# Kernel tuning notes

Measured on AMD Instinct MI355X. Metric: run time of the kernel, lower is better.

The kernel has to match this reference:

```python
import jax, jax.numpy as jnp
import numpy as np

HEAD_NUMS = 8
LN_EPS = 1e-5


def _layernorm(x, g, b):
    m = jnp.mean(x, axis=-1, keepdims=True)
    v = jnp.var(x, axis=-1, keepdims=True)
    return (x - m) * jax.lax.rsqrt(v + LN_EPS) * g + b


def setup_inputs() -> dict:
    key = jax.random.key(0)
    ks = jax.random.split(key, 6)
    B, S, D = 4, 2048, 512
    x = jax.random.normal(ks[0], (B, S, D), dtype=jnp.float32)
    W1 = jax.random.normal(ks[1], (4 * D, D), dtype=jnp.float32) * 0.02
    b1 = jnp.zeros((4 * D,), dtype=jnp.float32)
    ln_g = jnp.ones((D,), dtype=jnp.float32)
    ln_b = jnp.zeros((D,), dtype=jnp.float32)
    W2 = jax.random.normal(ks[2], (D, D), dtype=jnp.float32) * 0.02
    b2 = jnp.zeros((D,), dtype=jnp.float32)
    return {"x": x, "W1": W1, "b1": b1, "ln_g": ln_g, "ln_b": ln_b, "W2": W2, "b2": b2}


def reference(x, W1, b1, ln_g, ln_b, W2, b2):
    B, S, D = x.shape
    H = HEAD_NUMS
    hd = D // H
    # fused qkv+gate projection with SiLU (HSTU style)
    h = jax.nn.silu(x @ W1.T + b1)                   # [B,S,4D]
    h = h.reshape(B, S, 4, H, hd)                    # split into gate,q,k,v
    gate = jnp.transpose(h[:, :, 0], (0, 2, 1, 3))   # [B,H,S,hd]
    q = jnp.transpose(h[:, :, 1], (0, 2, 1, 3))
    k = jnp.transpose(h[:, :, 2], (0, 2, 1, 3))
    v = jnp.transpose(h[:, :, 3], (0, 2, 1, 3))
    scale = 1.0 / np.sqrt(hd).astype(np.float32)
    scores = jnp.einsum('bhsd,bhtd->bhst', q, k) * scale   # [B,H,S,S]
    causal = jnp.tril(jnp.ones((S, S), dtype=bool))        # allowed: t <= s
    # silu replaces softmax; masked (future) positions contribute 0
    # (mathematical limit of silu(-inf) is 0)
    a = jnp.where(causal, jax.nn.silu(scores), 0.0)
    o = jnp.einsum('bhst,bhtd->bhsd', a, v)                # [B,H,S,hd]
    o = jnp.transpose(o, (0, 2, 1, 3)).reshape(B, S, D)
    normed = _layernorm(o, ln_g, ln_b)
    gate_f = jnp.transpose(gate, (0, 2, 1, 3)).reshape(B, S, D)
    return (normed * gate_f) @ W2.T + b2
```

## Files before the change

### kernel.cpp

```cpp
#include <hip/hip_runtime.h>
#include <hip/hip_bf16.h>
#include <cstdint>


typedef __attribute__((ext_vector_type(8))) short short8;
typedef __attribute__((ext_vector_type(4))) float f32x4;

__device__ __forceinline__ unsigned short f2bf(float f) {
  union { float f; unsigned u; } v; v.f = f;
  unsigned r = v.u + 0x7FFFu + ((v.u >> 16) & 1u);
  return (unsigned short)(r >> 16);
}
__device__ __forceinline__ float bf2f(unsigned short h) {
  union { unsigned u; float f; } v; v.u = ((unsigned)h) << 16; return v.f;
}
__device__ __forceinline__ float fast_rcp(float x) {
#if __has_builtin(__builtin_amdgcn_rcpf)
  return __builtin_amdgcn_rcpf(x);
#else
  return 1.0f / x;
#endif
}
__device__ __forceinline__ float fast_exp2(float x) {
#if __has_builtin(__builtin_amdgcn_exp2f)
  return __builtin_amdgcn_exp2f(x);
#else
  return exp2f(x);
#endif
}
__device__ __forceinline__ float silu_f(float x) {
  return x * fast_rcp(1.0f + fast_exp2(-1.442695041f * x));
}
__device__ __forceinline__ unsigned pk2(float lo, float hi) {
  union { __hip_bfloat162 b; unsigned u; } cv;
  cv.b = __float22bfloat162_rn(make_float2(lo, hi));
  return cv.u;
}
__device__ __forceinline__ void gl_lds16(const void* g, void* l) {
  __builtin_amdgcn_global_load_lds(
      (const __attribute__((address_space(1))) void*)g,
      (__attribute__((address_space(3))) void*)l, 16, 0, 0);
}

__global__ void convert_kernel(const float* __restrict__ x, const float* __restrict__ w1,
                               const float* __restrict__ w2,
                               unsigned short* __restrict__ xb, unsigned short* __restrict__ w1b,
                               unsigned short* __restrict__ w2b) {
  int i = blockIdx.x * 256 + threadIdx.x;
  const float* s; unsigned short* d;
  if (i < 1048576) { s = x; d = xb; }
  else if (i < 1048576 + 262144) { i -= 1048576; s = w1; d = w1b; }
  else { i -= (1048576 + 262144); if (i >= 65536) return; s = w2; d = w2b; }
  float4 f = ((const float4*)s)[i];
  uint2 o; o.x = pk2(f.x, f.y); o.y = pk2(f.z, f.w);
  ((uint2*)d)[i] = o;
}

__global__ __launch_bounds__(256, 2) void gemm1_kernel(
    const unsigned short* __restrict__ xb,
    const unsigned short* __restrict__ w1b,
    const float* __restrict__ b1,
    unsigned short* __restrict__ h,
    unsigned short* __restrict__ vt)
{
  __shared__ __align__(16) unsigned short smem[16896];
  unsigned short* As = smem;
  unsigned short* Bs = smem + 8192;
  const int tid = threadIdx.x;
  const int w = tid >> 6, l = tid & 63;
  const int bm = blockIdx.x & 63, bn = blockIdx.x >> 6;
  const int wm = w & 1, wn = w >> 1;
  const int quad = l >> 4, lc = l & 15, lc7 = lc & 7;
  const int r8 = l >> 3, c8 = (l & 7) ^ r8;

  f32x4 acc[4][4] = {};
  const unsigned short* ga = xb + (size_t)(bm * 128 + w * 32 + r8) * 512 + c8 * 8;
  const unsigned short* gb = w1b + (size_t)(bn * 128 + w * 32 + r8) * 512 + c8 * 8;

  for (int kt = 0; kt < 512; kt += 64) {
#pragma unroll
    for (int i = 0; i < 4; ++i) {
      gl_lds16(ga + i * 8 * 512 + kt, As + (w * 4 + i) * 512);
      gl_lds16(gb + i * 8 * 512 + kt, Bs + (w * 4 + i) * 512);
    }
    __syncthreads();
#pragma unroll
    for (int kk = 0; kk < 2; ++kk) {
      short8 af[4], bf[4];
#pragma unroll
      for (int mt = 0; mt < 4; ++mt)
        af[mt] = *(const short8*)(As + (wm * 64 + mt * 16 + lc) * 64 +
                                  (((kk * 4 + quad) ^ lc7) * 8));
#pragma unroll
      for (int nt = 0; nt < 4; ++nt)
        bf[nt] = *(const short8*)(Bs + (wn * 64 + nt * 16 + lc) * 64 +
                                  (((kk * 4 + quad) ^ lc7) * 8));
#pragma unroll
      for (int mt = 0; mt < 4; ++mt)
#pragma unroll
        for (int nt = 0; nt < 4; ++nt)
          acc[mt][nt] = __builtin_amdgcn_mfma_f32_16x16x32_bf16(af[mt], bf[nt], acc[mt][nt], 0, 0, 0);
    }
    __syncthreads();
  }

  unsigned short* T = smem;
  const int sec = bn >> 2;
  if (sec == 3) {
#pragma unroll
    for (int nt = 0; nt < 4; ++nt) {
      const int nl = wn * 64 + nt * 16 + lc;
      const float bias = b1[bn * 128 + nl];
#pragma unroll
      for (int mt = 0; mt < 4; ++mt) {
        const int sl = wm * 64 + mt * 16 + quad * 4;
        uint2 pk;
        pk.x = pk2(silu_f(acc[mt][nt][0] + bias), silu_f(acc[mt][nt][1] + bias));
        pk.y = pk2(silu_f(acc[mt][nt][2] + bias), silu_f(acc[mt][nt][3] + bias));
        *(uint2*)(T + nl * 132 + sl) = pk;
      }
    }
  } else {
    const float osc = (sec == 1) ? 0.125f : 1.0f;
#pragma unroll
    for (int nt = 0; nt < 4; ++nt) {
      const int nl = wn * 64 + nt * 16 + lc;
      const float bias = b1[bn * 128 + nl];
#pragma unroll
      for (int mt = 0; mt < 4; ++mt) {
        const int sl = wm * 64 + mt * 16 + quad * 4;
#pragma unroll
        for (int r = 0; r < 4; ++r)
          T[(sl + r) * 132 + nl] = f2bf(silu_f(acc[mt][nt][r] + bias) * osc);
      }
    }
  }
  __syncthreads();
  const int rrow = tid >> 4, rcol = (tid & 15) * 8;
  if (sec == 3) {
    const int bq = bm >> 4, sbase = (bm & 15) * 128;
    const int lcq = tid & 15;
    const int t0 = ((lcq >> 2) * 32) + ((lcq & 3) * 4);
#pragma unroll
    for (int p = 0; p < 8; ++p) {
      const int row = p * 16 + rrow;
      const int n = bn * 128 + row, hh = (n >> 6) & 7, d = n & 63;
      uint2 a = *(const uint2*)(T + row * 132 + t0);
      uint2 bb = *(const uint2*)(T + row * 132 + t0 + 16);
      uint4 st; st.x = a.x; st.y = a.y; st.z = bb.x; st.w = bb.y;
      *(uint4*)(vt + (size_t)((bq * 8 + hh) * 64 + d) * 2048 + sbase + rcol) = st;
    }
  } else {
#pragma unroll
    for (int p = 0; p < 8; ++p) {
      const int row = p * 16 + rrow;
      *(short8*)(h + (size_t)(bm * 128 + row) * 2048 + bn * 128 + rcol) =
          *(const short8*)(T + row * 132 + rcol);
    }
  }
}

__global__ __launch_bounds__(256, 4) void attn_kernel(
    const unsigned short* __restrict__ h,
    const unsigned short* __restrict__ vt,
    float* __restrict__ o)
{
  __shared__ __align__(16) unsigned short Ks[128 * 64];
  __shared__ __align__(16) unsigned short Vs[64 * 128];
  const int tid = threadIdx.x;
  const int w = tid >> 6, l = tid & 63;
  const int bh = blockIdx.x & 31;
  const int qi = 31 - (blockIdx.x >> 5);
  const int b = bh >> 3, hh = bh & 7;
  const int quad = l >> 4, lc = l & 15, lc7 = lc & 7;
  const int r8 = l >> 3, c8 = (l & 7) ^ r8;
  const int q0 = qi * 64;
  const int nk = (qi >> 1) + 1;

  {
    const unsigned short* qg =
        h + (size_t)(b * 2048 + q0 + w * 16 + r8) * 2048 + 512 + hh * 64 + c8 * 8;
#pragma unroll
    for (int i = 0; i < 2; ++i)
      gl_lds16(qg + (size_t)i * 8 * 2048, Ks + (w * 2 + i) * 512);
  }
  __syncthreads();
  short8 qf[2];
#pragma unroll
  for (int kk = 0; kk < 2; ++kk)
    qf[kk] = *(const short8*)(Ks + (w * 16 + lc) * 64 + (((kk * 4 + quad) ^ lc7) * 8));

  f32x4 oacc[4] = {};

  const unsigned short* kg =
      h + (size_t)(b * 2048 + w * 32 + r8) * 2048 + 1024 + hh * 64 + c8 * 8;
  const int vrow = l >> 4, vcol = l & 15;
  const unsigned short* vgE =
      vt + (size_t)(bh * 64 + w * 16 + vrow) * 2048 + ((vcol ^ vrow) * 8);
  const unsigned short* vgO =
      vt + (size_t)(bh * 64 + w * 16 + vrow) * 2048 + ((vcol ^ vrow ^ 4) * 8);

  for (int ti = 0; ti < nk; ++ti) {
    __syncthreads();
    const int toff = ti * 128;
#pragma unroll
    for (int i = 0; i < 4; ++i) {
      gl_lds16(kg + (size_t)(toff + i * 8) * 2048, Ks + (w * 4 + i) * 512);
      const unsigned short* vsrc = ((i & 1) ? vgO : vgE) + (size_t)(i * 4) * 2048 + toff;
      gl_lds16(vsrc, Vs + (w * 4 + i) * 512);
    }
    __syncthreads();

    f32x4 sc[8] = {};
#pragma unroll
    for (int kk = 0; kk < 2; ++kk) {
#pragma unroll
      for (int mt = 0; mt < 8; ++mt) {
        short8 kf = *(const short8*)(Ks + (mt * 16 + lc) * 64 +
                                     (((kk * 4 + quad) ^ lc7) * 8));
        sc[mt] = __builtin_amdgcn_mfma_f32_16x16x32_bf16(kf, qf[kk], sc[mt], 0, 0, 0);
      }
    }

    if (ti < nk - 1) {
#pragma unroll
      for (int ks = 0; ks < 4; ++ks) {
        union { short8 s; unsigned u[4]; } pf;
        pf.u[0] = pk2(silu_f(sc[2 * ks][0]), silu_f(sc[2 * ks][1]));
        pf.u[1] = pk2(silu_f(sc[2 * ks][2]), silu_f(sc[2 * ks][3]));
        pf.u[2] = pk2(silu_f(sc[2 * ks + 1][0]), silu_f(sc[2 * ks + 1][1]));
        pf.u[3] = pk2(silu_f(sc[2 * ks + 1][2]), silu_f(sc[2 * ks + 1][3]));
#pragma unroll
        for (int nt = 0; nt < 4; ++nt) {
          short8 vf = *(const short8*)(Vs + (nt * 16 + lc) * 128 +
                                       (((ks * 4 + quad) ^ lc7) * 8));
          oacc[nt] = __builtin_amdgcn_mfma_f32_16x16x32_bf16(pf.s, vf, oacc[nt], 0, 0, 0);
        }
      }
    } else {
      const int qrow = q0 + w * 16 + lc;
#pragma unroll
      for (int ks = 0; ks < 4; ++ks) {
        float v[8];
#pragma unroll
        for (int g = 0; g < 2; ++g) {
          const int tb = toff + (2 * ks + g) * 16 + quad * 4;
#pragma unroll
          for (int r = 0; r < 4; ++r) {
            float s = silu_f(sc[2 * ks + g][r]);
            v[g * 4 + r] = (tb + r <= qrow) ? s : 0.0f;
          }
        }
        union { short8 s; unsigned u[4]; } pf;
        pf.u[0] = pk2(v[0], v[1]);
        pf.u[1] = pk2(v[2], v[3]);
        pf.u[2] = pk2(v[4], v[5]);
        pf.u[3] = pk2(v[6], v[7]);
#pragma unroll
        for (int nt = 0; nt < 4; ++nt) {
          short8 vf = *(const short8*)(Vs + (nt * 16 + lc) * 128 +
                                       (((ks * 4 + quad) ^ lc7) * 8));
          oacc[nt] = __builtin_amdgcn_mfma_f32_16x16x32_bf16(pf.s, vf, oacc[nt], 0, 0, 0);
        }
      }
    }
  }

  float* og = o + (size_t)(b * 2048 + q0 + w * 16) * 512 + hh * 64;
#pragma unroll
  for (int nt = 0; nt < 4; ++nt)
#pragma unroll
    for (int r = 0; r < 4; ++r)
      og[(quad * 4 + r) * 512 + nt * 16 + lc] = oacc[nt][r];
}

__global__ __launch_bounds__(256) void ln_gate_kernel(
    const float* __restrict__ o, const unsigned short* __restrict__ h,
    const float* __restrict__ lng, const float* __restrict__ lnb,
    unsigned short* __restrict__ y) {
  const int row = blockIdx.x * 4 + (threadIdx.x >> 6);
  const int l = threadIdx.x & 63;
  const float4* orow = (const float4*)(o + (size_t)row * 512);
  float4 a = orow[l * 2], c = orow[l * 2 + 1];
  float s0 = a.x + a.y + a.z + a.w + c.x + c.y + c.z + c.w;
#pragma unroll
  for (int off = 32; off > 0; off >>= 1) s0 += __shfl_xor(s0, off);
  const float mean = s0 * (1.0f / 512.0f);
  float dx[8] = {a.x - mean, a.y - mean, a.z - mean, a.w - mean,
                 c.x - mean, c.y - mean, c.z - mean, c.w - mean};
  float sq = 0.f;
#pragma unroll
  for (int j = 0; j < 8; ++j) sq += dx[j] * dx[j];
#pragma unroll
  for (int off = 32; off > 0; off >>= 1) sq += __shfl_xor(sq, off);
  const float inv = rsqrtf(sq * (1.0f / 512.0f) + 1e-5f);
  const float4* g4 = (const float4*)lng;
  const float4* b4 = (const float4*)lnb;
  float4 g0 = g4[l * 2], g1 = g4[l * 2 + 1], bb0 = b4[l * 2], bb1 = b4[l * 2 + 1];
  const unsigned short* grow = h + (size_t)row * 2048;
  ushort4 gr0 = *(const ushort4*)(grow + l * 8);
  ushort4 gr1 = *(const ushort4*)(grow + l * 8 + 4);
  float gg[8] = {g0.x, g0.y, g0.z, g0.w, g1.x, g1.y, g1.z, g1.w};
  float bbv[8] = {bb0.x, bb0.y, bb0.z, bb0.w, bb1.x, bb1.y, bb1.z, bb1.w};
  float gv[8] = {bf2f(gr0.x), bf2f(gr0.y), bf2f(gr0.z), bf2f(gr0.w),
                 bf2f(gr1.x), bf2f(gr1.y), bf2f(gr1.z), bf2f(gr1.w)};
  float r[8];
#pragma unroll
  for (int j = 0; j < 8; ++j) r[j] = (dx[j] * inv * gg[j] + bbv[j]) * gv[j];
  uint2 p0, p1;
  p0.x = pk2(r[0], r[1]); p0.y = pk2(r[2], r[3]);
  p1.x = pk2(r[4], r[5]); p1.y = pk2(r[6], r[7]);
  uint2* yrow = (uint2*)(y + (size_t)row * 512);
  yrow[l * 2] = p0;
  yrow[l * 2 + 1] = p1;
}

__global__ __launch_bounds__(256, 2) void gemm2_kernel(
    const unsigned short* __restrict__ yb,
    const unsigned short* __restrict__ w2b,
    const float* __restrict__ b2, float* __restrict__ out) {
  __shared__ __align__(16) unsigned short As[128 * 64];
  __shared__ __align__(16) unsigned short Bs[128 * 64];
  const int tid = threadIdx.x;
  const int w = tid >> 6, l = tid & 63;
  const int bm = blockIdx.x & 63, bn = blockIdx.x >> 6;
  const int wm = w & 1, wn = w >> 1;
  const int quad = l >> 4, lc = l & 15, lc7 = lc & 7;
  const int r8 = l >> 3, c8 = (l & 7) ^ r8;

  f32x4 acc[4][4] = {};
  const unsigned short* ga = yb + (size_t)(bm * 128 + w * 32 + r8) * 512 + c8 * 8;
  const unsigned short* gb = w2b + (size_t)(bn * 128 + w * 32 + r8) * 512 + c8 * 8;

  for (int kt = 0; kt < 512; kt += 64) {
#pragma unroll
    for (int i = 0; i < 4; ++i) {
      gl_lds16(ga + i * 8 * 512 + kt, As + (w * 4 + i) * 512);
      gl_lds16(gb + i * 8 * 512 + kt, Bs + (w * 4 + i) * 512);
    }
    __syncthreads();
#pragma unroll
    for (int kk = 0; kk < 2; ++kk) {
      short8 af[4], bf[4];
#pragma unroll
      for (int mt = 0; mt < 4; ++mt)
        af[mt] = *(const short8*)(As + (wm * 64 + mt * 16 + lc) * 64 +
                                  (((kk * 4 + quad) ^ lc7) * 8));
#pragma unroll
      for (int nt = 0; nt < 4; ++nt)
        bf[nt] = *(const short8*)(Bs + (wn * 64 + nt * 16 + lc) * 64 +
                                  (((kk * 4 + quad) ^ lc7) * 8));
#pragma unroll
      for (int mt = 0; mt < 4; ++mt)
#pragma unroll
        for (int nt = 0; nt < 4; ++nt)
          acc[mt][nt] = __builtin_amdgcn_mfma_f32_16x16x32_bf16(af[mt], bf[nt], acc[mt][nt], 0, 0, 0);
    }
    __syncthreads();
  }

#pragma unroll
  for (int nt = 0; nt < 4; ++nt) {
    const int n = bn * 128 + wn * 64 + nt * 16 + lc;
    const float bias = b2[n];
#pragma unroll
    for (int mt = 0; mt < 4; ++mt) {
      const int m0 = bm * 128 + wm * 64 + mt * 16 + quad * 4;
#pragma unroll
      for (int r = 0; r < 4; ++r)
        out[(size_t)(m0 + r) * 512 + n] = acc[mt][nt][r] + bias;
    }
  }
}

extern "C" void kernel_launch(void* const* d_in, const int* in_sizes, int n_in,
                              void* d_out, int out_size, void* d_ws, size_t ws_size,
                              hipStream_t stream) {
  const float* x = (const float*)d_in[0];
  const float* W1 = (const float*)d_in[1];
  const float* b1 = (const float*)d_in[2];
  const float* lng = (const float*)d_in[3];
  const float* lnb = (const float*)d_in[4];
  const float* W2 = (const float*)d_in[5];
  const float* b2 = (const float*)d_in[6];
  float* out = (float*)d_out;
  char* ws = (char*)d_ws;

  unsigned short* xb  = (unsigned short*)(ws);
  unsigned short* w1b = (unsigned short*)(ws + 8388608);
  unsigned short* w2b = (unsigned short*)(ws + 10485760);
  unsigned short* h   = (unsigned short*)(ws + 11010048);
  unsigned short* vt  = (unsigned short*)(ws + 44564480);
  float* o            = (float*)(ws + 52953088);
  unsigned short* yb  = (unsigned short*)(ws + 69730304);

  convert_kernel<<<5376, 256, 0, stream>>>(x, W1, W2, xb, w1b, w2b);
  gemm1_kernel<<<1024, 256, 0, stream>>>(xb, w1b, b1, h, vt);
  attn_kernel<<<1024, 256, 0, stream>>>(h, vt, o);
  ln_gate_kernel<<<2048, 256, 0, stream>>>(o, h, lng, lnb, yb);
  gemm2_kernel<<<256, 256, 0, stream>>>(yb, w2b, b2, out);
}
```

Baseline: 156.0 us.

## Pair causal query tiles per block and double-buffer K/V staging

Each attention block now processes two query tiles (qi = 31-p and p) so every block does the same 17 K/V tiles of work, which balances the causal triangle and halves the grid to 512 blocks. K and V tiles are double-buffered in shared memory, so the global-to-LDS copy of the next tile is issued before computing the current one, with one barrier per tile. The cost is twice the LDS footprint, plus a separate Q buffer, and launch bounds lowered from 4 to 2 blocks per SM, which reduces occupancy.

```diff
diff --git a/kernel.cpp b/kernel.cpp
--- a/kernel.cpp
+++ b/kernel.cpp
@@ -160,37 +160,24 @@
   }
 }
 
-__global__ __launch_bounds__(256, 4) void attn_kernel(
+__global__ __launch_bounds__(256, 2) void attn_kernel(
     const unsigned short* __restrict__ h,
     const unsigned short* __restrict__ vt,
     float* __restrict__ o)
 {
-  __shared__ __align__(16) unsigned short Ks[128 * 64];
-  __shared__ __align__(16) unsigned short Vs[64 * 128];
+  __shared__ __align__(16) unsigned short Qs[64 * 64];
+  __shared__ __align__(16) unsigned short Ks[2][128 * 64];
+  __shared__ __align__(16) unsigned short Vs[2][64 * 128];
   const int tid = threadIdx.x;
   const int w = tid >> 6, l = tid & 63;
   const int bh = blockIdx.x & 31;
-  const int qi = 31 - (blockIdx.x >> 5);
+  const int p = blockIdx.x >> 5;
   const int b = bh >> 3, hh = bh & 7;
   const int quad = l >> 4, lc = l & 15, lc7 = lc & 7;
   const int r8 = l >> 3, c8 = (l & 7) ^ r8;
-  const int q0 = qi * 64;
-  const int nk = (qi >> 1) + 1;
-
-  {
-    const unsigned short* qg =
-        h + (size_t)(b * 2048 + q0 + w * 16 + r8) * 2048 + 512 + hh * 64 + c8 * 8;
-#pragma unroll
-    for (int i = 0; i < 2; ++i)
-      gl_lds16(qg + (size_t)i * 8 * 2048, Ks + (w * 2 + i) * 512);
-  }
-  __syncthreads();
-  short8 qf[2];
-#pragma unroll
-  for (int kk = 0; kk < 2; ++kk)
-    qf[kk] = *(const short8*)(Ks + (w * 16 + lc) * 64 + (((kk * 4 + quad) ^ lc7) * 8));
-
-  f32x4 oacc[4] = {};
+  const int qiA = 31 - p, qiB = p;
+  const int q0A = qiA * 64, q0B = qiB * 64;
+  const int nkA = (qiA >> 1) + 1;
 
   const unsigned short* kg =
       h + (size_t)(b * 2048 + w * 32 + r8) * 2048 + 1024 + hh * 64 + c8 * 8;
@@ -200,29 +187,45 @@
   const unsigned short* vgO =
       vt + (size_t)(bh * 64 + w * 16 + vrow) * 2048 + ((vcol ^ vrow ^ 4) * 8);
 
-  for (int ti = 0; ti < nk; ++ti) {
-    __syncthreads();
-    const int toff = ti * 128;
+  auto stageQ = [&](int q0) {
+    const unsigned short* qg =
+        h + (size_t)(b * 2048 + q0 + w * 16 + r8) * 2048 + 512 + hh * 64 + c8 * 8;
+#pragma unroll
+    for (int i = 0; i < 2; ++i)
+      gl_lds16(qg + (size_t)i * 8 * 2048, Qs + (w * 2 + i) * 512);
+  };
+  auto stageKV = [&](int t, int pb) {
+    const int toff = t * 128;
 #pragma unroll
     for (int i = 0; i < 4; ++i) {
-      gl_lds16(kg + (size_t)(toff + i * 8) * 2048, Ks + (w * 4 + i) * 512);
+      gl_lds16(kg + (size_t)(toff + i * 8) * 2048, &Ks[pb][(w * 4 + i) * 512]);
       const unsigned short* vsrc = ((i & 1) ? vgO : vgE) + (size_t)(i * 4) * 2048 + toff;
-      gl_lds16(vsrc, Vs + (w * 4 + i) * 512);
-    }
-    __syncthreads();
-
+      gl_lds16(vsrc, &Vs[pb][(w * 4 + i) * 512]);
+    }
+  };
+
+  short8 qf[2];
+  auto readQ = [&]() {
+#pragma unroll
+    for (int kk = 0; kk < 2; ++kk)
+      qf[kk] = *(const short8*)(Qs + (w * 16 + lc) * 64 + (((kk * 4 + quad) ^ lc7) * 8));
+  };
+
+  f32x4 oacc[4] = {};
+
+  auto computeTile = [&](int pb, bool dg, int q0, int toff) {
+    const unsigned short* Kb = &Ks[pb][0];
+    const unsigned short* Vb = &Vs[pb][0];
     f32x4 sc[8] = {};
 #pragma unroll
-    for (int kk = 0; kk < 2; ++kk) {
+    for (int kk = 0; kk < 2; ++kk)
 #pragma unroll
       for (int mt = 0; mt < 8; ++mt) {
-        short8 kf = *(const short8*)(Ks + (mt * 16 + lc) * 64 +
+        short8 kf = *(const short8*)(Kb + (mt * 16 + lc) * 64 +
                                      (((kk * 4 + quad) ^ lc7) * 8));
         sc[mt] = __builtin_amdgcn_mfma_f32_16x16x32_bf16(kf, qf[kk], sc[mt], 0, 0, 0);
       }
-    }
-
-    if (ti < nk - 1) {
+    if (!dg) {
 #pragma unroll
       for (int ks = 0; ks < 4; ++ks) {
         union { short8 s; unsigned u[4]; } pf;
@@ -232,7 +235,7 @@
         pf.u[3] = pk2(silu_f(sc[2 * ks + 1][2]), silu_f(sc[2 * ks + 1][3]));
 #pragma unroll
         for (int nt = 0; nt < 4; ++nt) {
-          short8 vf = *(const short8*)(Vs + (nt * 16 + lc) * 128 +
+          short8 vf = *(const short8*)(Vb + (nt * 16 + lc) * 128 +
                                        (((ks * 4 + quad) ^ lc7) * 8));
           oacc[nt] = __builtin_amdgcn_mfma_f32_16x16x32_bf16(pf.s, vf, oacc[nt], 0, 0, 0);
         }
@@ -258,20 +261,61 @@
         pf.u[3] = pk2(v[6], v[7]);
 #pragma unroll
         for (int nt = 0; nt < 4; ++nt) {
-          short8 vf = *(const short8*)(Vs + (nt * 16 + lc) * 128 +
+          short8 vf = *(const short8*)(Vb + (nt * 16 + lc) * 128 +
                                        (((ks * 4 + quad) ^ lc7) * 8));
           oacc[nt] = __builtin_amdgcn_mfma_f32_16x16x32_bf16(pf.s, vf, oacc[nt], 0, 0, 0);
         }
       }
     }
-  }
-
-  float* og = o + (size_t)(b * 2048 + q0 + w * 16) * 512 + hh * 64;
-#pragma unroll
-  for (int nt = 0; nt < 4; ++nt)
-#pragma unroll
-    for (int r = 0; r < 4; ++r)
-      og[(quad * 4 + r) * 512 + nt * 16 + lc] = oacc[nt][r];
+  };
+
+  auto writeO = [&](int q0) {
+    float* og = o + (size_t)(b * 2048 + q0 + w * 16) * 512 + hh * 64;
+#pragma unroll
+    for (int nt = 0; nt < 4; ++nt)
+#pragma unroll
+      for (int r = 0; r < 4; ++r)
+        og[(quad * 4 + r) * 512 + nt * 16 + lc] = oacc[nt][r];
+  };
+
+  stageQ(q0A);
+  stageKV(0, 0);
+  __syncthreads();
+  readQ();
+
+#define CHUNK(c, PB)                                                          \
+  {                                                                          \
+    if ((c) == nkA) {                       \
+      writeO(q0A);                                                           \
+      _Pragma("unroll")                                                      \
+      for (int z = 0; z < 4; ++z) oacc[z] = (f32x4){0.f, 0.f, 0.f, 0.f};     \
+      readQ();                                                               \
+    }                                                                        \
+    {                                                                        \
+      const int nc = (c) + 1;                                                \
+      if (nc < 17) {                                                         \
+        const int ntile = (nc < nkA) ? nc : nc - nkA;                        \
+        stageKV(ntile, (PB) ^ 1);                                            \
+        if (nc == nkA) stageQ(q0B);                                          \
+      }                                                                      \
+    }                                                                        \
+    {                                                                        \
+      const int rel = ((c) < nkA) ? (c) : (c)-nkA;                           \
+      const bool dg = ((c) == nkA - 1) || ((c) == 16);                       \
+      const int q0c = ((c) < nkA) ? q0A : q0B;                               \
+      computeTile((PB), dg, q0c, rel * 128);                                 \
+    }                                                                        \
+    __syncthreads();                                                         \
+  }
+
+#pragma unroll 1
+  for (int c = 0; c < 16; c += 2) {
+    CHUNK(c, 0);
+    CHUNK(c + 1, 1);
+  }
+  CHUNK(16, 0);
+#undef CHUNK
+  writeO(q0B);
 }
 
 __global__ __launch_bounds__(256) void ln_gate_kernel(
@@ -396,7 +440,7 @@
 
   convert_kernel<<<5376, 256, 0, stream>>>(x, W1, W2, xb, w1b, w2b);
   gemm1_kernel<<<1024, 256, 0, stream>>>(xb, w1b, b1, h, vt);
-  attn_kernel<<<1024, 256, 0, stream>>>(h, vt, o);
+  attn_kernel<<<512, 256, 0, stream>>>(h, vt, o);
   ln_gate_kernel<<<2048, 256, 0, stream>>>(o, h, lng, lnb, yb);
   gemm2_kernel<<<256, 256, 0, stream>>>(yb, w2b, b2, out);
 }
```

Result: no change. 157.0 us (+0.6%).

## Use two-wave attention blocks with 32 query rows per wave and interleaved tile order

Applied to the files above, without the earlier changes.

The attention kernel now runs 128 threads per block instead of 256. Each wave handles two 16-row query sub-tiles, so every K and V fragment read from LDS feeds two MFMAs, and Q gets its own LDS buffer. The block-to-query-tile mapping interleaves short and long causal tiles across groups to balance work. The cost is more accumulator registers per wave, lower occupancy (launch bounds 128,2), and each wave loading twice as many K/V rows per step.

```diff
diff --git a/kernel.cpp b/kernel.cpp
--- a/kernel.cpp
+++ b/kernel.cpp
@@ -160,17 +160,22 @@
   }
 }
 
-__global__ __launch_bounds__(256, 4) void attn_kernel(
+__global__ __launch_bounds__(128, 2) void attn_kernel(
     const unsigned short* __restrict__ h,
     const unsigned short* __restrict__ vt,
     float* __restrict__ o)
 {
+  __shared__ __align__(16) unsigned short Qs[64 * 64];
   __shared__ __align__(16) unsigned short Ks[128 * 64];
   __shared__ __align__(16) unsigned short Vs[64 * 128];
   const int tid = threadIdx.x;
   const int w = tid >> 6, l = tid & 63;
-  const int bh = blockIdx.x & 31;
-  const int qi = 31 - (blockIdx.x >> 5);
+  const int r256 = blockIdx.x & 255, g = blockIdx.x >> 8;
+  const int bh = r256 & 31, tsel = r256 >> 5;
+  const int qi = (g == 0) ? 2 * tsel
+               : (g == 1) ? 2 * tsel + 1
+               : (g == 2) ? 30 - 2 * tsel
+                          : 31 - 2 * tsel;
   const int b = bh >> 3, hh = bh & 7;
   const int quad = l >> 4, lc = l & 15, lc7 = lc & 7;
   const int r8 = l >> 3, c8 = (l & 7) ^ r8;
@@ -179,99 +184,114 @@
 
   {
     const unsigned short* qg =
-        h + (size_t)(b * 2048 + q0 + w * 16 + r8) * 2048 + 512 + hh * 64 + c8 * 8;
-#pragma unroll
-    for (int i = 0; i < 2; ++i)
-      gl_lds16(qg + (size_t)i * 8 * 2048, Ks + (w * 2 + i) * 512);
+        h + (size_t)(b * 2048 + q0 + w * 32 + r8) * 2048 + 512 + hh * 64 + c8 * 8;
+#pragma unroll
+    for (int i = 0; i < 4; ++i)
+      gl_lds16(qg + (size_t)i * 8 * 2048, Qs + (w * 4 + i) * 512);
   }
   __syncthreads();
-  short8 qf[2];
-#pragma unroll
-  for (int kk = 0; kk < 2; ++kk)
-    qf[kk] = *(const short8*)(Ks + (w * 16 + lc) * 64 + (((kk * 4 + quad) ^ lc7) * 8));
-
-  f32x4 oacc[4] = {};
+  short8 qf[2][2];
+#pragma unroll
+  for (int s = 0; s < 2; ++s)
+#pragma unroll
+    for (int kk = 0; kk < 2; ++kk)
+      qf[s][kk] = *(const short8*)(Qs + (w * 32 + s * 16 + lc) * 64 +
+                                   (((kk * 4 + quad) ^ lc7) * 8));
+
+  f32x4 oacc[2][4] = {};
 
   const unsigned short* kg =
-      h + (size_t)(b * 2048 + w * 32 + r8) * 2048 + 1024 + hh * 64 + c8 * 8;
+      h + (size_t)(b * 2048 + w * 64 + r8) * 2048 + 1024 + hh * 64 + c8 * 8;
   const int vrow = l >> 4, vcol = l & 15;
   const unsigned short* vgE =
-      vt + (size_t)(bh * 64 + w * 16 + vrow) * 2048 + ((vcol ^ vrow) * 8);
+      vt + (size_t)(bh * 64 + w * 32 + vrow) * 2048 + ((vcol ^ vrow) * 8);
   const unsigned short* vgO =
-      vt + (size_t)(bh * 64 + w * 16 + vrow) * 2048 + ((vcol ^ vrow ^ 4) * 8);
+      vt + (size_t)(bh * 64 + w * 32 + vrow) * 2048 + ((vcol ^ vrow ^ 4) * 8);
 
   for (int ti = 0; ti < nk; ++ti) {
     __syncthreads();
     const int toff = ti * 128;
 #pragma unroll
-    for (int i = 0; i < 4; ++i) {
-      gl_lds16(kg + (size_t)(toff + i * 8) * 2048, Ks + (w * 4 + i) * 512);
+    for (int i = 0; i < 8; ++i) {
+      gl_lds16(kg + (size_t)(toff + i * 8) * 2048, Ks + (w * 8 + i) * 512);
       const unsigned short* vsrc = ((i & 1) ? vgO : vgE) + (size_t)(i * 4) * 2048 + toff;
-      gl_lds16(vsrc, Vs + (w * 4 + i) * 512);
-    }
-    __syncthreads();
-
-    f32x4 sc[8] = {};
-#pragma unroll
-    for (int kk = 0; kk < 2; ++kk) {
+      gl_lds16(vsrc, Vs + (w * 8 + i) * 512);
+    }
+    __syncthreads();
+
+    f32x4 sc[2][8] = {};
+#pragma unroll
+    for (int kk = 0; kk < 2; ++kk)
 #pragma unroll
       for (int mt = 0; mt < 8; ++mt) {
         short8 kf = *(const short8*)(Ks + (mt * 16 + lc) * 64 +
                                      (((kk * 4 + quad) ^ lc7) * 8));
-        sc[mt] = __builtin_amdgcn_mfma_f32_16x16x32_bf16(kf, qf[kk], sc[mt], 0, 0, 0);
+        sc[0][mt] = __builtin_amdgcn_mfma_f32_16x16x32_bf16(kf, qf[0][kk], sc[0][mt], 0, 0, 0);
+        sc[1][mt] = __builtin_amdgcn_mfma_f32_16x16x32_bf16(kf, qf[1][kk], sc[1][mt], 0, 0, 0);
       }
-    }
 
     if (ti < nk - 1) {
 #pragma unroll
       for (int ks = 0; ks < 4; ++ks) {
-        union { short8 s; unsigned u[4]; } pf;
-        pf.u[0] = pk2(silu_f(sc[2 * ks][0]), silu_f(sc[2 * ks][1]));
-        pf.u[1] = pk2(silu_f(sc[2 * ks][2]), silu_f(sc[2 * ks][3]));
-        pf.u[2] = pk2(silu_f(sc[2 * ks + 1][0]), silu_f(sc[2 * ks + 1][1]));
-        pf.u[3] = pk2(silu_f(sc[2 * ks + 1][2]), silu_f(sc[2 * ks + 1][3]));
+        union { short8 s; unsigned u[4]; } pf0, pf1;
+        pf0.u[0] = pk2(silu_f(sc[0][2 * ks][0]), silu_f(sc[0][2 * ks][1]));
+        pf0.u[1] = pk2(silu_f(sc[0][2 * ks][2]), silu_f(sc[0][2 * ks][3]));
+        pf0.u[2] = pk2(silu_f(sc[0][2 * ks + 1][0]), silu_f(sc[0][2 * ks + 1][1]));
+        pf0.u[3] = pk2(silu_f(sc[0][2 * ks + 1][2]), silu_f(sc[0][2 * ks + 1][3]));
+        pf1.u[0] = pk2(silu_f(sc[1][2 * ks][0]), silu_f(sc[1][2 * ks][1]));
+        pf1.u[1] = pk2(silu_f(sc[1][2 * ks][2]), silu_f(sc[1][2 * ks][3]));
+        pf1.u[2] = pk2(silu_f(sc[1][2 * ks + 1][0]), silu_f(sc[1][2 * ks + 1][1]));
+        pf1.u[3] = pk2(silu_f(sc[1][2 * ks + 1][2]), silu_f(sc[1][2 * ks + 1][3]));
 #pragma unroll
         for (int nt = 0; nt < 4; ++nt) {
           short8 vf = *(const short8*)(Vs + (nt * 16 + lc) * 128 +
                                        (((ks * 4 + quad) ^ lc7) * 8));
-          oacc[nt] = __builtin_amdgcn_mfma_f32_16x16x32_bf16(pf.s, vf, oacc[nt], 0, 0, 0);
+          oacc[0][nt] = __builtin_amdgcn_mfma_f32_16x16x32_bf16(pf0.s, vf, oacc[0][nt], 0, 0, 0);
+          oacc[1][nt] = __builtin_amdgcn_mfma_f32_16x16x32_bf16(pf1.s, vf, oacc[1][nt], 0, 0, 0);
         }
       }
     } else {
-      const int qrow = q0 + w * 16 + lc;
+      const int qrow0 = q0 + w * 32 + lc;
+      const int qrow1 = qrow0 + 16;
 #pragma unroll
       for (int ks = 0; ks < 4; ++ks) {
-        float v[8];
-#pragma unroll
-        for (int g = 0; g < 2; ++g) {
-          const int tb = toff + (2 * ks + g) * 16 + quad * 4;
+        float v0[8], v1[8];
+#pragma unroll
+        for (int gg = 0; gg < 2; ++gg) {
+          const int tb = toff + (2 * ks + gg) * 16 + quad * 4;
 #pragma unroll
           for (int r = 0; r < 4; ++r) {
-            float s = silu_f(sc[2 * ks + g][r]);
-            v[g * 4 + r] = (tb + r <= qrow) ? s : 0.0f;
+            float s0 = silu_f(sc[0][2 * ks + gg][r]);
+            float s1 = silu_f(sc[1][2 * ks + gg][r]);
+            v0[gg * 4 + r] = (tb + r <= qrow0) ? s0 : 0.0f;
+            v1[gg * 4 + r] = (tb + r <= qrow1) ? s1 : 0.0f;
           }
         }
-        union { short8 s; unsigned u[4]; } pf;
-        pf.u[0] = pk2(v[0], v[1]);
-        pf.u[1] = pk2(v[2], v[3]);
-        pf.u[2] = pk2(v[4], v[5]);
-        pf.u[3] = pk2(v[6], v[7]);
+        union { short8 s; unsigned u[4]; } pf0, pf1;
+        pf0.u[0] = pk2(v0[0], v0[1]); pf0.u[1] = pk2(v0[2], v0[3]);
+        pf0.u[2] = pk2(v0[4], v0[5]); pf0.u[3] = pk2(v0[6], v0[7]);
+        pf1.u[0] = pk2(v1[0], v1[1]); pf1.u[1] = pk2(v1[2], v1[3]);
+        pf1.u[2] = pk2(v1[4], v1[5]); pf1.u[3] = pk2(v1[6], v1[7]);
 #pragma unroll
         for (int nt = 0; nt < 4; ++nt) {
           short8 vf = *(const short8*)(Vs + (nt * 16 + lc) * 128 +
                                        (((ks * 4 + quad) ^ lc7) * 8));
-          oacc[nt] = __builtin_amdgcn_mfma_f32_16x16x32_bf16(pf.s, vf, oacc[nt], 0, 0, 0);
+          oacc[0][nt] = __builtin_amdgcn_mfma_f32_16x16x32_bf16(pf0.s, vf, oacc[0][nt], 0, 0, 0);
+          oacc[1][nt] = __builtin_amdgcn_mfma_f32_16x16x32_bf16(pf1.s, vf, oacc[1][nt], 0, 0, 0);
         }
       }
     }
   }
 
-  float* og = o + (size_t)(b * 2048 + q0 + w * 16) * 512 + hh * 64;
-#pragma unroll
-  for (int nt = 0; nt < 4; ++nt)
-#pragma unroll
-    for (int r = 0; r < 4; ++r)
-      og[(quad * 4 + r) * 512 + nt * 16 + lc] = oacc[nt][r];
+#pragma unroll
+  for (int s = 0; s < 2; ++s) {
+    float* og = o + (size_t)(b * 2048 + q0 + w * 32 + s * 16) * 512 + hh * 64;
+#pragma unroll
+    for (int nt = 0; nt < 4; ++nt)
+#pragma unroll
+      for (int r = 0; r < 4; ++r)
+        og[(quad * 4 + r) * 512 + nt * 16 + lc] = oacc[s][nt][r];
+  }
 }
 
 __global__ __launch_bounds__(256) void ln_gate_kernel(
@@ -396,7 +416,7 @@
 
   convert_kernel<<<5376, 256, 0, stream>>>(x, W1, W2, xb, w1b, w2b);
   gemm1_kernel<<<1024, 256, 0, stream>>>(xb, w1b, b1, h, vt);
-  attn_kernel<<<1024, 256, 0, stream>>>(h, vt, o);
+  attn_kernel<<<1024, 128, 0, stream>>>(h, vt, o);
   ln_gate_kernel<<<2048, 256, 0, stream>>>(o, h, lng, lnb, yb);
   gemm2_kernel<<<256, 256, 0, stream>>>(yb, w2b, b2, out);
 }
```

After: 180.5 us. 1.16x slower.

## Balance causal attention work by splitting long query tiles and pairing with short ones

Applied to the files above, without the earlier changes.

The attention kernel now gives each block an equal amount of KV work. Half the blocks process the first 8 KV tiles of a long query tile. The other half finish the rest of that tile into a separate partial buffer and then process a short query tile. The partial sums are added in the layernorm kernel. Separately, the output GEMM uses 128x64 tiles and 512 blocks instead of 256 to fill more CUs. This reuses the xb workspace region for the partial buffer, which is safe only because xb is dead after gemm1.

```diff
diff --git a/kernel.cpp b/kernel.cpp
--- a/kernel.cpp
+++ b/kernel.cpp
@@ -163,34 +163,21 @@
 __global__ __launch_bounds__(256, 4) void attn_kernel(
     const unsigned short* __restrict__ h,
     const unsigned short* __restrict__ vt,
-    float* __restrict__ o)
+    float* __restrict__ o,
+    float* __restrict__ o1)
 {
   __shared__ __align__(16) unsigned short Ks[128 * 64];
   __shared__ __align__(16) unsigned short Vs[64 * 128];
   const int tid = threadIdx.x;
   const int w = tid >> 6, l = tid & 63;
   const int bh = blockIdx.x & 31;
-  const int qi = 31 - (blockIdx.x >> 5);
+  const int job = blockIdx.x >> 5;
+  const int p = job >> 1, hf = job & 1;
   const int b = bh >> 3, hh = bh & 7;
   const int quad = l >> 4, lc = l & 15, lc7 = lc & 7;
   const int r8 = l >> 3, c8 = (l & 7) ^ r8;
-  const int q0 = qi * 64;
-  const int nk = (qi >> 1) + 1;
-
-  {
-    const unsigned short* qg =
-        h + (size_t)(b * 2048 + q0 + w * 16 + r8) * 2048 + 512 + hh * 64 + c8 * 8;
-#pragma unroll
-    for (int i = 0; i < 2; ++i)
-      gl_lds16(qg + (size_t)i * 8 * 2048, Ks + (w * 2 + i) * 512);
-  }
-  __syncthreads();
-  short8 qf[2];
-#pragma unroll
-  for (int kk = 0; kk < 2; ++kk)
-    qf[kk] = *(const short8*)(Ks + (w * 16 + lc) * 64 + (((kk * 4 + quad) ^ lc7) * 8));
-
-  f32x4 oacc[4] = {};
+  const int qiA = 31 - p;
+  const int nkA = (qiA >> 1) + 1;
 
   const unsigned short* kg =
       h + (size_t)(b * 2048 + w * 32 + r8) * 2048 + 1024 + hh * 64 + c8 * 8;
@@ -200,8 +187,22 @@
   const unsigned short* vgO =
       vt + (size_t)(bh * 64 + w * 16 + vrow) * 2048 + ((vcol ^ vrow ^ 4) * 8);
 
-  for (int ti = 0; ti < nk; ++ti) {
-    __syncthreads();
+  short8 qf[2];
+  f32x4 oacc[4] = {};
+
+  auto stageQ = [&](int q0) {
+    const unsigned short* qg =
+        h + (size_t)(b * 2048 + q0 + w * 16 + r8) * 2048 + 512 + hh * 64 + c8 * 8;
+#pragma unroll
+    for (int i = 0; i < 2; ++i)
+      gl_lds16(qg + (size_t)i * 8 * 2048, Ks + (w * 2 + i) * 512);
+  };
+  auto readQ = [&]() {
+#pragma unroll
+    for (int kk = 0; kk < 2; ++kk)
+      qf[kk] = *(const short8*)(Ks + (w * 16 + lc) * 64 + (((kk * 4 + quad) ^ lc7) * 8));
+  };
+  auto stageKV = [&](int ti) {
     const int toff = ti * 128;
 #pragma unroll
     for (int i = 0; i < 4; ++i) {
@@ -209,20 +210,18 @@
       const unsigned short* vsrc = ((i & 1) ? vgO : vgE) + (size_t)(i * 4) * 2048 + toff;
       gl_lds16(vsrc, Vs + (w * 4 + i) * 512);
     }
-    __syncthreads();
-
+  };
+  auto computeTile = [&](bool dg, int q0, int toff) {
     f32x4 sc[8] = {};
 #pragma unroll
-    for (int kk = 0; kk < 2; ++kk) {
+    for (int kk = 0; kk < 2; ++kk)
 #pragma unroll
       for (int mt = 0; mt < 8; ++mt) {
         short8 kf = *(const short8*)(Ks + (mt * 16 + lc) * 64 +
                                      (((kk * 4 + quad) ^ lc7) * 8));
         sc[mt] = __builtin_amdgcn_mfma_f32_16x16x32_bf16(kf, qf[kk], sc[mt], 0, 0, 0);
       }
-    }
-
-    if (ti < nk - 1) {
+    if (!dg) {
 #pragma unroll
       for (int ks = 0; ks < 4; ++ks) {
         union { short8 s; unsigned u[4]; } pf;
@@ -264,24 +263,74 @@
         }
       }
     }
-  }
-
-  float* og = o + (size_t)(b * 2048 + q0 + w * 16) * 512 + hh * 64;
-#pragma unroll
-  for (int nt = 0; nt < 4; ++nt)
-#pragma unroll
-    for (int r = 0; r < 4; ++r)
-      og[(quad * 4 + r) * 512 + nt * 16 + lc] = oacc[nt][r];
+  };
+  auto writeO = [&](float* base) {
+#pragma unroll
+    for (int nt = 0; nt < 4; ++nt)
+#pragma unroll
+      for (int r = 0; r < 4; ++r)
+        base[(quad * 4 + r) * 512 + nt * 16 + lc] = oacc[nt][r];
+  };
+
+  if (hf == 0) {
+    const int q0 = qiA * 64;
+    stageQ(q0);
+    __syncthreads();
+    readQ();
+    for (int ti = 0; ti < 8; ++ti) {
+      __syncthreads();
+      stageKV(ti);
+      __syncthreads();
+      computeTile(false, q0, ti * 128);
+    }
+    writeO(o + (size_t)(b * 2048 + q0 + w * 16) * 512 + hh * 64);
+  } else {
+    const int q0 = qiA * 64;
+    stageQ(q0);
+    __syncthreads();
+    readQ();
+    for (int ti = 8; ti < nkA; ++ti) {
+      __syncthreads();
+      stageKV(ti);
+      __syncthreads();
+      computeTile(ti == nkA - 1, q0, ti * 128);
+    }
+    writeO(o1 + (size_t)(b * 1024 + (q0 - 1024) + w * 16) * 512 + hh * 64);
+#pragma unroll
+    for (int z = 0; z < 4; ++z) oacc[z] = (f32x4){0.f, 0.f, 0.f, 0.f};
+    __syncthreads();
+    const int q0B = p * 64;
+    const int nkB = 17 - nkA;
+    stageQ(q0B);
+    __syncthreads();
+    readQ();
+    for (int ti = 0; ti < nkB; ++ti) {
+      __syncthreads();
+      stageKV(ti);
+      __syncthreads();
+      computeTile(ti == nkB - 1, q0B, ti * 128);
+    }
+    writeO(o + (size_t)(b * 2048 + q0B + w * 16) * 512 + hh * 64);
+  }
 }
 
 __global__ __launch_bounds__(256) void ln_gate_kernel(
-    const float* __restrict__ o, const unsigned short* __restrict__ h,
+    const float* __restrict__ o, const float* __restrict__ o1,
+    const unsigned short* __restrict__ h,
     const float* __restrict__ lng, const float* __restrict__ lnb,
     unsigned short* __restrict__ y) {
   const int row = blockIdx.x * 4 + (threadIdx.x >> 6);
   const int l = threadIdx.x & 63;
   const float4* orow = (const float4*)(o + (size_t)row * 512);
   float4 a = orow[l * 2], c = orow[l * 2 + 1];
+  const int s = row & 2047;
+  if (s >= 1024) {
+    const float4* o1row =
+        (const float4*)(o1 + (size_t)((row >> 11) * 1024 + (s - 1024)) * 512);
+    float4 a1 = o1row[l * 2], c1 = o1row[l * 2 + 1];
+    a.x += a1.x; a.y += a1.y; a.z += a1.z; a.w += a1.w;
+    c.x += c1.x; c.y += c1.y; c.z += c1.z; c.w += c1.w;
+  }
   float s0 = a.x + a.y + a.z + a.w + c.x + c.y + c.z + c.w;
 #pragma unroll
   for (int off = 32; off > 0; off >>= 1) s0 += __shfl_xor(s0, off);
@@ -320,7 +369,7 @@
     const unsigned short* __restrict__ w2b,
     const float* __restrict__ b2, float* __restrict__ out) {
   __shared__ __align__(16) unsigned short As[128 * 64];
-  __shared__ __align__(16) unsigned short Bs[128 * 64];
+  __shared__ __align__(16) unsigned short Bs[64 * 64];
   const int tid = threadIdx.x;
   const int w = tid >> 6, l = tid & 63;
   const int bm = blockIdx.x & 63, bn = blockIdx.x >> 6;
@@ -328,40 +377,41 @@
   const int quad = l >> 4, lc = l & 15, lc7 = lc & 7;
   const int r8 = l >> 3, c8 = (l & 7) ^ r8;
 
-  f32x4 acc[4][4] = {};
+  f32x4 acc[4][2] = {};
   const unsigned short* ga = yb + (size_t)(bm * 128 + w * 32 + r8) * 512 + c8 * 8;
-  const unsigned short* gb = w2b + (size_t)(bn * 128 + w * 32 + r8) * 512 + c8 * 8;
+  const unsigned short* gb = w2b + (size_t)(bn * 64 + w * 16 + r8) * 512 + c8 * 8;
 
   for (int kt = 0; kt < 512; kt += 64) {
 #pragma unroll
-    for (int i = 0; i < 4; ++i) {
+    for (int i = 0; i < 4; ++i)
       gl_lds16(ga + i * 8 * 512 + kt, As + (w * 4 + i) * 512);
-      gl_lds16(gb + i * 8 * 512 + kt, Bs + (w * 4 + i) * 512);
-    }
+#pragma unroll
+    for (int i = 0; i < 2; ++i)
+      gl_lds16(gb + i * 8 * 512 + kt, Bs + (w * 2 + i) * 512);
     __syncthreads();
 #pragma unroll
     for (int kk = 0; kk < 2; ++kk) {
-      short8 af[4], bf[4];
+      short8 af[4], bf[2];
 #pragma unroll
       for (int mt = 0; mt < 4; ++mt)
         af[mt] = *(const short8*)(As + (wm * 64 + mt * 16 + lc) * 64 +
                                   (((kk * 4 + quad) ^ lc7) * 8));
 #pragma unroll
-      for (int nt = 0; nt < 4; ++nt)
-        bf[nt] = *(const short8*)(Bs + (wn * 64 + nt * 16 + lc) * 64 +
+      for (int nt = 0; nt < 2; ++nt)
+        bf[nt] = *(const short8*)(Bs + (wn * 32 + nt * 16 + lc) * 64 +
                                   (((kk * 4 + quad) ^ lc7) * 8));
 #pragma unroll
       for (int mt = 0; mt < 4; ++mt)
 #pragma unroll
-        for (int nt = 0; nt < 4; ++nt)
+        for (int nt = 0; nt < 2; ++nt)
           acc[mt][nt] = __builtin_amdgcn_mfma_f32_16x16x32_bf16(af[mt], bf[nt], acc[mt][nt], 0, 0, 0);
     }
     __syncthreads();
   }
 
 #pragma unroll
-  for (int nt = 0; nt < 4; ++nt) {
-    const int n = bn * 128 + wn * 64 + nt * 16 + lc;
+  for (int nt = 0; nt < 2; ++nt) {
+    const int n = bn * 64 + wn * 32 + nt * 16 + lc;
     const float bias = b2[n];
 #pragma unroll
     for (int mt = 0; mt < 4; ++mt) {
@@ -393,10 +443,11 @@
   unsigned short* vt  = (unsigned short*)(ws + 44564480);
   float* o            = (float*)(ws + 52953088);
   unsigned short* yb  = (unsigned short*)(ws + 69730304);
+  float* o1           = (float*)(ws);
 
   convert_kernel<<<5376, 256, 0, stream>>>(x, W1, W2, xb, w1b, w2b);
   gemm1_kernel<<<1024, 256, 0, stream>>>(xb, w1b, b1, h, vt);
-  attn_kernel<<<1024, 256, 0, stream>>>(h, vt, o);
-  ln_gate_kernel<<<2048, 256, 0, stream>>>(o, h, lng, lnb, yb);
-  gemm2_kernel<<<256, 256, 0, stream>>>(yb, w2b, b2, out);
-}
+  attn_kernel<<<1024, 256, 0, stream>>>(h, vt, o, o1);
+  ln_gate_kernel<<<2048, 256, 0, stream>>>(o, o1, h, lng, lnb, yb);
+  gemm2_kernel<<<512, 256, 0, stream>>>(yb, w2b, b2, out);
+}
```

Measured after the change: 173.5 us. +11.2%, slower.
